# Kernel tuning notes

Hardware: AMD Instinct MI355X
Metric: run time of the kernel (lower is better)

Reference implementation:

```python
import jax, jax.numpy as jnp
import numpy as np

E = 1024
H = 16
D = E // H  # head_dim = 64
B, L, S = 2, 2048, 2048


def setup_inputs() -> dict:
    key = jax.random.key(0)
    ks = jax.random.split(key, 10)
    scale = 1.0 / np.sqrt(E)
    return {
        "x": jax.random.normal(ks[0], (B, L, E), jnp.float32),
        "context": jax.random.normal(ks[1], (B, S, E), jnp.float32),
        "Wq": jax.random.normal(ks[2], (E, E), jnp.float32) * scale,
        "bq": jnp.zeros((E,), jnp.float32),
        "Wk": jax.random.normal(ks[3], (E, E), jnp.float32) * scale,
        "bk": jnp.zeros((E,), jnp.float32),
        "Wv": jax.random.normal(ks[4], (E, E), jnp.float32) * scale,
        "bv": jnp.zeros((E,), jnp.float32),
        "Wp": jax.random.normal(ks[5], (E, E), jnp.float32) * scale,
        "bp": jnp.zeros((E,), jnp.float32),
    }


def reference(x, context, Wq, bq, Wk, bk, Wv, bv, Wp, bp):
    b, l, _ = x.shape
    s = context.shape[1]
    # linear projections then split heads: [B, H, L/S, D]
    q = (x @ Wq + bq).reshape(b, l, H, D).transpose(0, 2, 1, 3)
    k = (context @ Wk + bk).reshape(b, s, H, D).transpose(0, 2, 1, 3)
    v = (context @ Wv + bv).reshape(b, s, H, D).transpose(0, 2, 1, 3)
    # scores [B, H, L, S]
    attn = jnp.einsum("bhld,bhsd->bhls", q, k) / jnp.sqrt(jnp.float32(D))
    attn = jax.nn.softmax(attn, axis=-1)
    # dropout is identity in eval mode
    out = jnp.einsum("bhls,bhsd->bhld", attn, v)
    out = out.transpose(0, 2, 1, 3).reshape(b, l, E)
    return out @ Wp + bp
```

## Files before the change

### kernel.cpp

```cpp
#include <hip/hip_runtime.h>
#include <math.h>

#define B_ 2
#define L_ 2048
#define S_ 2048
#define E_ 1024
#define H_ 16
#define D_ 64
#define SC_ 0.180336880111120f

typedef unsigned short u16;
typedef unsigned int u32;
typedef __attribute__((ext_vector_type(8))) short short8;
typedef __attribute__((ext_vector_type(4))) float floatx4;

__device__ __forceinline__ u16 f2bf(float f) {
    union { float f; unsigned u; } a; a.f = f;
    unsigned r = a.u + 0x7FFFu + ((a.u >> 16) & 1u);
    return (u16)(r >> 16);
}

__device__ __forceinline__ u32 cvt_pk_bf16(float lo, float hi) {
    u32 d;
    asm("v_cvt_pk_bf16_f32 %0, %1, %2" : "=v"(d) : "v"(lo), "v"(hi));
    return d;
}

__device__ __forceinline__ void glds16(const u16* g, u16* l) {
    __builtin_amdgcn_global_load_lds(
        (const __attribute__((address_space(1))) void*)g,
        (__attribute__((address_space(3))) void*)l, 16, 0, 0);
}

__global__ void cast_bf16_kernel(const float* __restrict__ x, const float* __restrict__ ctx,
                                 u16* __restrict__ Xb, u16* __restrict__ Cb) {
    const float* src = blockIdx.y ? ctx : x;
    u16* dst = blockIdx.y ? Cb : Xb;
    int i = blockIdx.x * 256 + threadIdx.x;
    float4 u0 = ((const float4*)src)[2 * i];
    float4 u1 = ((const float4*)src)[2 * i + 1];
    uint4 o;
    o.x = f2bf(u0.x) | ((unsigned)f2bf(u0.y) << 16);
    o.y = f2bf(u0.z) | ((unsigned)f2bf(u0.w) << 16);
    o.z = f2bf(u1.x) | ((unsigned)f2bf(u1.y) << 16);
    o.w = f2bf(u1.z) | ((unsigned)f2bf(u1.w) << 16);
    ((uint4*)dst)[i] = o;
}

__global__ void transpose_cast_kernel(const float* __restrict__ Wq, const float* __restrict__ Wk,
                                      const float* __restrict__ Wv, const float* __restrict__ Wp,
                                      u16* __restrict__ WqT, u16* __restrict__ WkT,
                                      u16* __restrict__ WvT, u16* __restrict__ WpT) {
    const int z = blockIdx.z;
    const float* W = z == 0 ? Wq : (z == 1 ? Wk : (z == 2 ? Wv : Wp));
    u16* Wt = z == 0 ? WqT : (z == 1 ? WkT : (z == 2 ? WvT : WpT));
    __shared__ float tile[32][33];
    const int bx = blockIdx.x * 32, by = blockIdx.y * 32;
    const int tx = threadIdx.x, ty = threadIdx.y;
#pragma unroll
    for (int j = 0; j < 4; ++j)
        tile[ty + j * 8][tx] = W[(size_t)(by + ty + j * 8) * E_ + bx + tx];
    __syncthreads();
#pragma unroll
    for (int j = 0; j < 4; ++j)
        Wt[(size_t)(bx + ty + j * 8) * E_ + by + tx] = f2bf(tile[tx][ty + j * 8]);
}

__global__ __launch_bounds__(256, 3) void qkv_gemm_kernel(
    const u16* __restrict__ Xb, const u16* __restrict__ Cb,
    const u16* __restrict__ WqT, const u16* __restrict__ WkT, const u16* __restrict__ WvT,
    const float* __restrict__ bq, const float* __restrict__ bk, const float* __restrict__ bv,
    u16* __restrict__ Qb, u16* __restrict__ Kb, u16* __restrict__ Vtb) {
    __shared__ __align__(16) u16 As[128 * 64];
    __shared__ __align__(16) u16 Bs[128 * 64];

    const int z = blockIdx.z;
    const u16* A  = z == 0 ? Xb : Cb;
    const u16* Bt = z == 0 ? WqT : (z == 1 ? WkT : WvT);
    const float* bias = z == 0 ? bq : (z == 1 ? bk : bv);
    const float scale = z == 0 ? SC_ : 1.0f;

    const int tid = threadIdx.x;
    const int lane = tid & 63;
    const int wv = tid >> 6;
    const int wm = wv >> 1, wn = wv & 1;
    const int qd = lane >> 4, lr = lane & 15;
    const int m0 = blockIdx.y * 128, n0 = blockIdx.x * 128;
    const int lrow = lane >> 3;
    const int gu = (lane & 7) ^ lrow;

    floatx4 acc[4][4];
#pragma unroll
    for (int i = 0; i < 4; ++i)
#pragma unroll
        for (int j = 0; j < 4; ++j) {
            floatx4 zz = {0.f, 0.f, 0.f, 0.f};
            acc[i][j] = zz;
        }

#pragma unroll
    for (int j = 0; j < 4; ++j) {
        int c = wv * 4 + j;
        glds16(A  + (size_t)(m0 + c * 8 + lrow) * E_ + gu * 8, &As[c * 512]);
        glds16(Bt + (size_t)(n0 + c * 8 + lrow) * E_ + gu * 8, &Bs[c * 512]);
    }
    __syncthreads();

    for (int t = 0; t < 16; ++t) {
        short8 af[4][2], bf[4][2];
#pragma unroll
        for (int mi = 0; mi < 4; ++mi)
#pragma unroll
            for (int kk = 0; kk < 2; ++kk) {
                int row = wm * 64 + mi * 16 + lr;
                int u = (kk * 4 + qd) ^ (lr & 7);
                af[mi][kk] = *(const short8*)(&As[row * 64 + u * 8]);
            }
#pragma unroll
        for (int ni = 0; ni < 4; ++ni)
#pragma unroll
            for (int kk = 0; kk < 2; ++kk) {
                int row = wn * 64 + ni * 16 + lr;
                int u = (kk * 4 + qd) ^ (lr & 7);
                bf[ni][kk] = *(const short8*)(&Bs[row * 64 + u * 8]);
            }
#pragma unroll
        for (int kk = 0; kk < 2; ++kk)
#pragma unroll
            for (int mi = 0; mi < 4; ++mi)
#pragma unroll
                for (int ni = 0; ni < 4; ++ni)
                    acc[mi][ni] = __builtin_amdgcn_mfma_f32_16x16x32_bf16(
                        af[mi][kk], bf[ni][kk], acc[mi][ni], 0, 0, 0);
        __syncthreads();
        if (t + 1 < 16) {
            int kb = (t + 1) * 64;
#pragma unroll
            for (int j = 0; j < 4; ++j) {
                int c = wv * 4 + j;
                glds16(A  + (size_t)(m0 + c * 8 + lrow) * E_ + kb + gu * 8, &As[c * 512]);
                glds16(Bt + (size_t)(n0 + c * 8 + lrow) * E_ + kb + gu * 8, &Bs[c * 512]);
            }
        }
        __syncthreads();
    }

    u16* Cq = z == 0 ? Qb : Kb;
#pragma unroll
    for (int mi = 0; mi < 4; ++mi) {
#pragma unroll
        for (int ni = 0; ni < 4; ++ni) {
            int col = n0 + wn * 64 + ni * 16 + lr;
            float bv_ = bias[col];
            if (z == 2) {
                int row0 = m0 + wm * 64 + mi * 16 + qd * 4;
                int bidx = row0 >> 11;
                int sloc = row0 & (S_ - 1);
                u16 h0 = f2bf(acc[mi][ni][0] + bv_);
                u16 h1 = f2bf(acc[mi][ni][1] + bv_);
                u16 h2 = f2bf(acc[mi][ni][2] + bv_);
                u16 h3 = f2bf(acc[mi][ni][3] + bv_);
                uint2 pk;
                pk.x = h0 | ((unsigned)h1 << 16);
                pk.y = h2 | ((unsigned)h3 << 16);
                *(uint2*)&Vtb[((size_t)(bidx * E_ + col)) * S_ + sloc] = pk;
            } else {
#pragma unroll
                for (int r = 0; r < 4; ++r) {
                    int row = m0 + wm * 64 + mi * 16 + qd * 4 + r;
                    Cq[(size_t)row * E_ + col] = f2bf((acc[mi][ni][r] + bv_) * scale);
                }
            }
        }
    }
}

#define PSTR 68

__global__ __launch_bounds__(256, 4) void flash_attn_kernel(
    const u16* __restrict__ Q, const u16* __restrict__ Kg,
    const u16* __restrict__ Vtg, u16* __restrict__ Opart, float* __restrict__ lpart) {
    __shared__ __align__(16) u16 Ps[128 * PSTR];
    __shared__ __align__(16) u16 Ks[64 * 64];
    __shared__ __align__(16) u16 Vs[64 * 64];

    const int tid = threadIdx.x;
    const int lane = tid & 63;
    const int wv = tid >> 6;
    const int qd = lane >> 4, lr = lane & 15;
    const int b = blockIdx.y >> 4, h = blockIdx.y & 15;
    const int q0 = blockIdx.x * 128;
    const int z = blockIdx.z;
    const int sbeg = z * (S_ / 2);

    u16* Op = Opart + (size_t)z * (B_ * L_ * E_);
    float* lp = lpart + (size_t)z * (B_ * H_ * L_);

    const u16* Qbase = Q + (size_t)(b * L_ + q0) * E_ + h * D_;
    const u16* Kbase = Kg + (size_t)(b * S_) * E_ + h * D_;
    const u16* Vbase = Vtg + (size_t)(b * E_ + h * D_) * S_;

    const int srow = tid >> 3;
    const int scol = (tid & 7) * 8;
    const int lrow = lane >> 3;
    const int gu = (lane & 7) ^ lrow;

#pragma unroll
    for (int j = 0; j < 2; ++j) {
        int c = wv * 2 + j;
        glds16(Kbase + (size_t)(sbeg + c * 8 + lrow) * E_ + gu * 8, &Ks[c * 512]);
        glds16(Vbase + (size_t)(c * 8 + lrow) * S_ + sbeg + gu * 8, &Vs[c * 512]);
    }

#pragma unroll
    for (int c = 0; c < 4; ++c) {
        int row = srow + c * 32;
        *(uint4*)(&Ps[row * PSTR + scol]) = *(const uint4*)(Qbase + (size_t)row * E_ + scol);
    }
    __syncthreads();

    short8 qf[2][2];
#pragma unroll
    for (int mi = 0; mi < 2; ++mi)
#pragma unroll
        for (int kk = 0; kk < 2; ++kk)
            qf[mi][kk] = *(const short8*)(&Ps[(wv * 32 + mi * 16 + lr) * PSTR + kk * 32 + qd * 8]);

    floatx4 o_acc[2][4];
    float l_acc[2][4];
#pragma unroll
    for (int mi = 0; mi < 2; ++mi)
#pragma unroll
        for (int nt = 0; nt < 4; ++nt) {
            floatx4 z4 = {0.f, 0.f, 0.f, 0.f};
            o_acc[mi][nt] = z4;
        }
#pragma unroll
    for (int mi = 0; mi < 2; ++mi)
#pragma unroll
        for (int r = 0; r < 4; ++r) l_acc[mi][r] = 0.f;

    const int NIT = (S_ / 2) / 64;

    for (int it = 0; it < NIT; ++it) {
        floatx4 s_[2][4];
#pragma unroll
        for (int nt = 0; nt < 4; ++nt) {
            int krow = nt * 16 + lr;
            short8 kb0 = *(const short8*)(&Ks[krow * 64 + ((qd) ^ (lr & 7)) * 8]);
            short8 kb1 = *(const short8*)(&Ks[krow * 64 + ((4 + qd) ^ (lr & 7)) * 8]);
#pragma unroll
            for (int mi = 0; mi < 2; ++mi) {
                floatx4 zz = {0.f, 0.f, 0.f, 0.f};
                zz = __builtin_amdgcn_mfma_f32_16x16x32_bf16(qf[mi][0], kb0, zz, 0, 0, 0);
                zz = __builtin_amdgcn_mfma_f32_16x16x32_bf16(qf[mi][1], kb1, zz, 0, 0, 0);
                s_[mi][nt] = zz;
            }
        }

#pragma unroll
        for (int mi = 0; mi < 2; ++mi)
#pragma unroll
            for (int nt = 0; nt < 4; ++nt)
#pragma unroll
                for (int r = 0; r < 4; ++r) {
                    float p = __builtin_amdgcn_exp2f(s_[mi][nt][r]);
                    l_acc[mi][r] += p;
                    Ps[(wv * 32 + mi * 16 + qd * 4 + r) * PSTR + nt * 16 + lr] = f2bf(p);
                }
        asm volatile("s_waitcnt lgkmcnt(0)" ::: "memory");

        short8 pf[2][2];
#pragma unroll
        for (int mi = 0; mi < 2; ++mi)
#pragma unroll
            for (int kk = 0; kk < 2; ++kk)
                pf[mi][kk] = *(const short8*)(&Ps[(wv * 32 + mi * 16 + lr) * PSTR + kk * 32 + qd * 8]);
#pragma unroll
        for (int nt = 0; nt < 4; ++nt) {
            int vrow = nt * 16 + lr;
            short8 vb0 = *(const short8*)(&Vs[vrow * 64 + ((qd) ^ (lr & 7)) * 8]);
            short8 vb1 = *(const short8*)(&Vs[vrow * 64 + ((4 + qd) ^ (lr & 7)) * 8]);
#pragma unroll
            for (int mi = 0; mi < 2; ++mi) {
                o_acc[mi][nt] = __builtin_amdgcn_mfma_f32_16x16x32_bf16(pf[mi][0], vb0, o_acc[mi][nt], 0, 0, 0);
                o_acc[mi][nt] = __builtin_amdgcn_mfma_f32_16x16x32_bf16(pf[mi][1], vb1, o_acc[mi][nt], 0, 0, 0);
            }
        }

        __syncthreads();
        if (it + 1 < NIT) {
            int s1 = sbeg + (it + 1) * 64;
#pragma unroll
            for (int j = 0; j < 2; ++j) {
                int c = wv * 2 + j;
                glds16(Kbase + (size_t)(s1 + c * 8 + lrow) * E_ + gu * 8, &Ks[c * 512]);
                glds16(Vbase + (size_t)(c * 8 + lrow) * S_ + s1 + gu * 8, &Vs[c * 512]);
            }
            __syncthreads();
        }
    }

    float linv[2][4];
#pragma unroll
    for (int mi = 0; mi < 2; ++mi)
#pragma unroll
        for (int r = 0; r < 4; ++r) {
            float l = l_acc[mi][r];
#pragma unroll
            for (int st = 1; st < 16; st <<= 1) l += __shfl_xor(l, st);
            if (lr == 0)
                lp[(size_t)(b * H_ + h) * L_ + q0 + wv * 32 + mi * 16 + qd * 4 + r] = l;
            linv[mi][r] = 1.0f / l;
        }

#pragma unroll
    for (int mi = 0; mi < 2; ++mi)
#pragma unroll
        for (int nt = 0; nt < 4; ++nt)
#pragma unroll
            for (int r = 0; r < 4; ++r) {
                int row = q0 + wv * 32 + mi * 16 + qd * 4 + r;
                int col = h * D_ + nt * 16 + lr;
                Op[(size_t)(b * L_ + row) * E_ + col] = f2bf(o_acc[mi][nt][r] * linv[mi][r]);
            }
}

__global__ __launch_bounds__(256, 2) void out_gemm_kernel(
    const u16* __restrict__ O1, const u16* __restrict__ O2,
    const float* __restrict__ l1, const float* __restrict__ l2,
    const u16* __restrict__ WpT, const float* __restrict__ bp,
    float* __restrict__ out) {
    __shared__ __align__(16) u16 As[128 * 64];
    __shared__ __align__(16) u16 Bs[128 * 64];

    const int tid = threadIdx.x;
    const int lane = tid & 63;
    const int wv = tid >> 6;
    const int wm = wv >> 1, wn = wv & 1;
    const int qd = lane >> 4, lr = lane & 15;
    const int m0 = blockIdx.y * 128, n0 = blockIdx.x * 128;
    const int lrow = lane >> 3;
    const int gu = (lane & 7) ^ lrow;

    floatx4 acc[4][4];
#pragma unroll
    for (int i = 0; i < 4; ++i)
#pragma unroll
        for (int j = 0; j < 4; ++j) {
            floatx4 zz = {0.f, 0.f, 0.f, 0.f};
            acc[i][j] = zz;
        }

#define STAGE_A(tt)                                                                   \
    {                                                                                 \
        int col = (tt)*64 + gu * 8;                                                   \
        _Pragma("unroll") for (int j = 0; j < 4; ++j) {                               \
            int c = wv * 4 + j;                                                       \
            int row = m0 + c * 8 + lrow;                                              \
            uint4 a1 = *(const uint4*)(O1 + (size_t)row * E_ + col);                  \
            uint4 a2 = *(const uint4*)(O2 + (size_t)row * E_ + col);                  \
            int li = (row >> 11) * (H_ * L_) + (tt)*L_ + (row & (L_ - 1));            \
            float la = l1[li], lb = l2[li];                                           \
            float s = 1.0f / (la + lb);                                               \
            float w1 = la * s, w2 = lb * s;                                           \
            const u32* pa = (const u32*)&a1;                                          \
            const u32* pb = (const u32*)&a2;                                          \
            uint4 o;                                                                  \
            u32* po = (u32*)&o;                                                       \
            _Pragma("unroll") for (int d = 0; d < 4; ++d) {                           \
                union { u32 u; float f; } x0, x1, y0, y1;                             \
                x0.u = pa[d] << 16; x1.u = pa[d] & 0xFFFF0000u;                       \
                y0.u = pb[d] << 16; y1.u = pb[d] & 0xFFFF0000u;                       \
                po[d] = cvt_pk_bf16(x0.f * w1 + y0.f * w2, x1.f * w1 + y1.f * w2);    \
            }                                                                         \
            *(uint4*)(&As[c * 512 + lane * 8]) = o;                                   \
        }                                                                             \
    }

#pragma unroll
    for (int j = 0; j < 4; ++j) {
        int c = wv * 4 + j;
        glds16(WpT + (size_t)(n0 + c * 8 + lrow) * E_ + gu * 8, &Bs[c * 512]);
    }
    STAGE_A(0)
    __syncthreads();

    for (int t = 0; t < 16; ++t) {
        short8 af[4][2], bf[4][2];
#pragma unroll
        for (int mi = 0; mi < 4; ++mi)
#pragma unroll
            for (int kk = 0; kk < 2; ++kk) {
                int row = wm * 64 + mi * 16 + lr;
                int u = (kk * 4 + qd) ^ (lr & 7);
                af[mi][kk] = *(const short8*)(&As[row * 64 + u * 8]);
            }
#pragma unroll
        for (int ni = 0; ni < 4; ++ni)
#pragma unroll
            for (int kk = 0; kk < 2; ++kk) {
                int row = wn * 64 + ni * 16 + lr;
                int u = (kk * 4 + qd) ^ (lr & 7);
                bf[ni][kk] = *(const short8*)(&Bs[row * 64 + u * 8]);
            }
#pragma unroll
        for (int kk = 0; kk < 2; ++kk)
#pragma unroll
            for (int mi = 0; mi < 4; ++mi)
#pragma unroll
                for (int ni = 0; ni < 4; ++ni)
                    acc[mi][ni] = __builtin_amdgcn_mfma_f32_16x16x32_bf16(
                        af[mi][kk], bf[ni][kk], acc[mi][ni], 0, 0, 0);
        __syncthreads();
        if (t + 1 < 16) {
            int kb = (t + 1) * 64;
#pragma unroll
            for (int j = 0; j < 4; ++j) {
                int c = wv * 4 + j;
                glds16(WpT + (size_t)(n0 + c * 8 + lrow) * E_ + kb + gu * 8, &Bs[c * 512]);
            }
            STAGE_A(t + 1)
        }
        __syncthreads();
    }

#pragma unroll
    for (int mi = 0; mi < 4; ++mi)
#pragma unroll
        for (int ni = 0; ni < 4; ++ni) {
            int col = n0 + wn * 64 + ni * 16 + lr;
            float bv_ = bp[col];
#pragma unroll
            for (int r = 0; r < 4; ++r) {
                int row = m0 + wm * 64 + mi * 16 + qd * 4 + r;
                out[(size_t)row * E_ + col] = acc[mi][ni][r] + bv_;
            }
        }
}

extern "C" void kernel_launch(void* const* d_in, const int* in_sizes, int n_in,
                              void* d_out, int out_size, void* d_ws, size_t ws_size,
                              hipStream_t stream) {
    const float* x   = (const float*)d_in[0];
    const float* ctx = (const float*)d_in[1];
    const float* Wq  = (const float*)d_in[2];
    const float* bq  = (const float*)d_in[3];
    const float* Wk  = (const float*)d_in[4];
    const float* bk  = (const float*)d_in[5];
    const float* Wv  = (const float*)d_in[6];
    const float* bv  = (const float*)d_in[7];
    const float* Wp  = (const float*)d_in[8];
    const float* bp  = (const float*)d_in[9];
    float* out = (float*)d_out;

    u16* WqT = (u16*)d_ws;
    u16* WkT = WqT + 1048576;
    u16* WvT = WkT + 1048576;
    u16* WpT = WvT + 1048576;
    u16* Qb  = WpT + 1048576;
    u16* Kb  = Qb + 4194304;
    u16* Vtb = Kb + 4194304;
    u16* Xb  = Vtb + 4194304;
    u16* Cb  = Xb + 4194304;
    u16* Opart = Xb;
    float* lpart = (float*)(Cb + 4194304);
    (void)ws_size; (void)in_sizes; (void)n_in; (void)out_size;

    cast_bf16_kernel<<<dim3(2048, 2), 256, 0, stream>>>(x, ctx, Xb, Cb);
    transpose_cast_kernel<<<dim3(32, 32, 4), dim3(32, 8), 0, stream>>>(
        Wq, Wk, Wv, Wp, WqT, WkT, WvT, WpT);

    qkv_gemm_kernel<<<dim3(8, 32, 3), 256, 0, stream>>>(
        Xb, Cb, WqT, WkT, WvT, bq, bk, bv, Qb, Kb, Vtb);

    flash_attn_kernel<<<dim3(L_ / 128, B_ * H_, 2), 256, 0, stream>>>(
        Qb, Kb, Vtb, Opart, lpart);

    out_gemm_kernel<<<dim3(8, 32), 256, 0, stream>>>(
        Opart, Opart + 4194304, lpart, lpart + B_ * H_ * L_, WpT, bp, out);
}
```

Measured before the change: 242.4 us.

## Double-buffer LDS tiles in all GEMM and attention kernels, fuse input cast into QKV

Drops the separate fp32-to-bf16 cast kernel for x and context. The QKV GEMM now reads fp32 activations directly into registers and converts them into a double-buffered LDS tile. The QKV GEMM, flash attention and output GEMM all move to two LDS buffers, so the next tile's loads are issued before the current tile's MFMAs, and each iteration needs one barrier instead of two. This trades larger LDS and register footprint (occupancy hints lowered from 3→2 and 4→3) for overlap of memory with compute and one fewer kernel launch and round trip through global memory.

```diff
diff --git a/kernel.cpp b/kernel.cpp
--- a/kernel.cpp
+++ b/kernel.cpp
@@ -30,21 +30,6 @@
     __builtin_amdgcn_global_load_lds(
         (const __attribute__((address_space(1))) void*)g,
         (__attribute__((address_space(3))) void*)l, 16, 0, 0);
-}
-
-__global__ void cast_bf16_kernel(const float* __restrict__ x, const float* __restrict__ ctx,
-                                 u16* __restrict__ Xb, u16* __restrict__ Cb) {
-    const float* src = blockIdx.y ? ctx : x;
-    u16* dst = blockIdx.y ? Cb : Xb;
-    int i = blockIdx.x * 256 + threadIdx.x;
-    float4 u0 = ((const float4*)src)[2 * i];
-    float4 u1 = ((const float4*)src)[2 * i + 1];
-    uint4 o;
-    o.x = f2bf(u0.x) | ((unsigned)f2bf(u0.y) << 16);
-    o.y = f2bf(u0.z) | ((unsigned)f2bf(u0.w) << 16);
-    o.z = f2bf(u1.x) | ((unsigned)f2bf(u1.y) << 16);
-    o.w = f2bf(u1.z) | ((unsigned)f2bf(u1.w) << 16);
-    ((uint4*)dst)[i] = o;
 }
 
 __global__ void transpose_cast_kernel(const float* __restrict__ Wq, const float* __restrict__ Wk,
@@ -66,16 +51,16 @@
         Wt[(size_t)(bx + ty + j * 8) * E_ + by + tx] = f2bf(tile[tx][ty + j * 8]);
 }
 
-__global__ __launch_bounds__(256, 3) void qkv_gemm_kernel(
-    const u16* __restrict__ Xb, const u16* __restrict__ Cb,
+__global__ __launch_bounds__(256, 2) void qkv_gemm_kernel(
+    const float* __restrict__ x, const float* __restrict__ ctx,
     const u16* __restrict__ WqT, const u16* __restrict__ WkT, const u16* __restrict__ WvT,
     const float* __restrict__ bq, const float* __restrict__ bk, const float* __restrict__ bv,
     u16* __restrict__ Qb, u16* __restrict__ Kb, u16* __restrict__ Vtb) {
-    __shared__ __align__(16) u16 As[128 * 64];
-    __shared__ __align__(16) u16 Bs[128 * 64];
+    __shared__ __align__(16) u16 As[2][128 * 64];
+    __shared__ __align__(16) u16 Bs[2][128 * 64];
 
     const int z = blockIdx.z;
-    const u16* A  = z == 0 ? Xb : Cb;
+    const float* A  = z == 0 ? x : ctx;
     const u16* Bt = z == 0 ? WqT : (z == 1 ? WkT : WvT);
     const float* bias = z == 0 ? bq : (z == 1 ? bk : bv);
     const float scale = z == 0 ? SC_ : 1.0f;
@@ -88,6 +73,8 @@
     const int m0 = blockIdx.y * 128, n0 = blockIdx.x * 128;
     const int lrow = lane >> 3;
     const int gu = (lane & 7) ^ lrow;
+    const int arow = tid >> 3;
+    const int au = tid & 7;
 
     floatx4 acc[4][4];
 #pragma unroll
@@ -98,15 +85,51 @@
             acc[i][j] = zz;
         }
 
-#pragma unroll
-    for (int j = 0; j < 4; ++j) {
-        int c = wv * 4 + j;
-        glds16(A  + (size_t)(m0 + c * 8 + lrow) * E_ + gu * 8, &As[c * 512]);
-        glds16(Bt + (size_t)(n0 + c * 8 + lrow) * E_ + gu * 8, &Bs[c * 512]);
-    }
+    float4 av[4][2];
+
+#define LOAD_A(kb)                                                                 \
+    {                                                                              \
+        _Pragma("unroll") for (int c2 = 0; c2 < 4; ++c2) {                         \
+            const float* src = A + (size_t)(m0 + arow + c2 * 32) * E_ + (kb) + au * 8; \
+            av[c2][0] = *(const float4*)src;                                       \
+            av[c2][1] = *(const float4*)(src + 4);                                 \
+        }                                                                          \
+    }
+
+#define WRITE_A(buf)                                                               \
+    {                                                                              \
+        _Pragma("unroll") for (int c2 = 0; c2 < 4; ++c2) {                         \
+            int row = arow + c2 * 32;                                              \
+            uint4 o;                                                               \
+            o.x = cvt_pk_bf16(av[c2][0].x, av[c2][0].y);                           \
+            o.y = cvt_pk_bf16(av[c2][0].z, av[c2][0].w);                           \
+            o.z = cvt_pk_bf16(av[c2][1].x, av[c2][1].y);                           \
+            o.w = cvt_pk_bf16(av[c2][1].z, av[c2][1].w);                           \
+            *(uint4*)(&As[buf][row * 64 + (au ^ (row & 7)) * 8]) = o;              \
+        }                                                                          \
+    }
+
+#define STAGE_B(buf, kb)                                                           \
+    {                                                                              \
+        _Pragma("unroll") for (int j = 0; j < 4; ++j) {                            \
+            int c = wv * 4 + j;                                                    \
+            glds16(Bt + (size_t)(n0 + c * 8 + lrow) * E_ + (kb) + gu * 8,          \
+                   &Bs[buf][c * 512]);                                             \
+        }                                                                          \
+    }
+
+    LOAD_A(0)
+    STAGE_B(0, 0)
+    WRITE_A(0)
     __syncthreads();
 
     for (int t = 0; t < 16; ++t) {
+        const int cur = t & 1;
+        if (t + 1 < 16) {
+            STAGE_B(cur ^ 1, (t + 1) * 64)
+            LOAD_A((t + 1) * 64)
+        }
+
         short8 af[4][2], bf[4][2];
 #pragma unroll
         for (int mi = 0; mi < 4; ++mi)
@@ -114,7 +137,7 @@
             for (int kk = 0; kk < 2; ++kk) {
                 int row = wm * 64 + mi * 16 + lr;
                 int u = (kk * 4 + qd) ^ (lr & 7);
-                af[mi][kk] = *(const short8*)(&As[row * 64 + u * 8]);
+                af[mi][kk] = *(const short8*)(&As[cur][row * 64 + u * 8]);
             }
 #pragma unroll
         for (int ni = 0; ni < 4; ++ni)
@@ -122,7 +145,7 @@
             for (int kk = 0; kk < 2; ++kk) {
                 int row = wn * 64 + ni * 16 + lr;
                 int u = (kk * 4 + qd) ^ (lr & 7);
-                bf[ni][kk] = *(const short8*)(&Bs[row * 64 + u * 8]);
+                bf[ni][kk] = *(const short8*)(&Bs[cur][row * 64 + u * 8]);
             }
 #pragma unroll
         for (int kk = 0; kk < 2; ++kk)
@@ -132,16 +155,8 @@
                 for (int ni = 0; ni < 4; ++ni)
                     acc[mi][ni] = __builtin_amdgcn_mfma_f32_16x16x32_bf16(
                         af[mi][kk], bf[ni][kk], acc[mi][ni], 0, 0, 0);
-        __syncthreads();
-        if (t + 1 < 16) {
-            int kb = (t + 1) * 64;
-#pragma unroll
-            for (int j = 0; j < 4; ++j) {
-                int c = wv * 4 + j;
-                glds16(A  + (size_t)(m0 + c * 8 + lrow) * E_ + kb + gu * 8, &As[c * 512]);
-                glds16(Bt + (size_t)(n0 + c * 8 + lrow) * E_ + kb + gu * 8, &Bs[c * 512]);
-            }
-        }
+
+        if (t + 1 < 16) WRITE_A(cur ^ 1)
         __syncthreads();
     }
 
@@ -173,16 +188,19 @@
             }
         }
     }
+#undef LOAD_A
+#undef WRITE_A
+#undef STAGE_B
 }
 
 #define PSTR 68
 
-__global__ __launch_bounds__(256, 4) void flash_attn_kernel(
+__global__ __launch_bounds__(256, 3) void flash_attn_kernel(
     const u16* __restrict__ Q, const u16* __restrict__ Kg,
     const u16* __restrict__ Vtg, u16* __restrict__ Opart, float* __restrict__ lpart) {
     __shared__ __align__(16) u16 Ps[128 * PSTR];
-    __shared__ __align__(16) u16 Ks[64 * 64];
-    __shared__ __align__(16) u16 Vs[64 * 64];
+    __shared__ __align__(16) u16 Ks[2][64 * 64];
+    __shared__ __align__(16) u16 Vs[2][64 * 64];
 
     const int tid = threadIdx.x;
     const int lane = tid & 63;
@@ -208,8 +226,8 @@
 #pragma unroll
     for (int j = 0; j < 2; ++j) {
         int c = wv * 2 + j;
-        glds16(Kbase + (size_t)(sbeg + c * 8 + lrow) * E_ + gu * 8, &Ks[c * 512]);
-        glds16(Vbase + (size_t)(c * 8 + lrow) * S_ + sbeg + gu * 8, &Vs[c * 512]);
+        glds16(Kbase + (size_t)(sbeg + c * 8 + lrow) * E_ + gu * 8, &Ks[0][c * 512]);
+        glds16(Vbase + (size_t)(c * 8 + lrow) * S_ + sbeg + gu * 8, &Vs[0][c * 512]);
     }
 
 #pragma unroll
@@ -243,12 +261,23 @@
     const int NIT = (S_ / 2) / 64;
 
     for (int it = 0; it < NIT; ++it) {
+        const int cur = it & 1;
+        if (it + 1 < NIT) {
+            int s1 = sbeg + (it + 1) * 64;
+#pragma unroll
+            for (int j = 0; j < 2; ++j) {
+                int c = wv * 2 + j;
+                glds16(Kbase + (size_t)(s1 + c * 8 + lrow) * E_ + gu * 8, &Ks[cur ^ 1][c * 512]);
+                glds16(Vbase + (size_t)(c * 8 + lrow) * S_ + s1 + gu * 8, &Vs[cur ^ 1][c * 512]);
+            }
+        }
+
         floatx4 s_[2][4];
 #pragma unroll
         for (int nt = 0; nt < 4; ++nt) {
             int krow = nt * 16 + lr;
-            short8 kb0 = *(const short8*)(&Ks[krow * 64 + ((qd) ^ (lr & 7)) * 8]);
-            short8 kb1 = *(const short8*)(&Ks[krow * 64 + ((4 + qd) ^ (lr & 7)) * 8]);
+            short8 kb0 = *(const short8*)(&Ks[cur][krow * 64 + ((qd) ^ (lr & 7)) * 8]);
+            short8 kb1 = *(const short8*)(&Ks[cur][krow * 64 + ((4 + qd) ^ (lr & 7)) * 8]);
 #pragma unroll
             for (int mi = 0; mi < 2; ++mi) {
                 floatx4 zz = {0.f, 0.f, 0.f, 0.f};
@@ -279,8 +308,8 @@
 #pragma unroll
         for (int nt = 0; nt < 4; ++nt) {
             int vrow = nt * 16 + lr;
-            short8 vb0 = *(const short8*)(&Vs[vrow * 64 + ((qd) ^ (lr & 7)) * 8]);
-            short8 vb1 = *(const short8*)(&Vs[vrow * 64 + ((4 + qd) ^ (lr & 7)) * 8]);
+            short8 vb0 = *(const short8*)(&Vs[cur][vrow * 64 + ((qd) ^ (lr & 7)) * 8]);
+            short8 vb1 = *(const short8*)(&Vs[cur][vrow * 64 + ((4 + qd) ^ (lr & 7)) * 8]);
 #pragma unroll
             for (int mi = 0; mi < 2; ++mi) {
                 o_acc[mi][nt] = __builtin_amdgcn_mfma_f32_16x16x32_bf16(pf[mi][0], vb0, o_acc[mi][nt], 0, 0, 0);
@@ -289,16 +318,6 @@
         }
 
         __syncthreads();
-        if (it + 1 < NIT) {
-            int s1 = sbeg + (it + 1) * 64;
-#pragma unroll
-            for (int j = 0; j < 2; ++j) {
-                int c = wv * 2 + j;
-                glds16(Kbase + (size_t)(s1 + c * 8 + lrow) * E_ + gu * 8, &Ks[c * 512]);
-                glds16(Vbase + (size_t)(c * 8 + lrow) * S_ + s1 + gu * 8, &Vs[c * 512]);
-            }
-            __syncthreads();
-        }
     }
 
     float linv[2][4];
@@ -331,8 +350,8 @@
     const float* __restrict__ l1, const float* __restrict__ l2,
     const u16* __restrict__ WpT, const float* __restrict__ bp,
     float* __restrict__ out) {
-    __shared__ __align__(16) u16 As[128 * 64];
-    __shared__ __align__(16) u16 Bs[128 * 64];
+    __shared__ __align__(16) u16 As[2][128 * 64];
+    __shared__ __align__(16) u16 Bs[2][128 * 64];
 
     const int tid = threadIdx.x;
     const int lane = tid & 63;
@@ -352,41 +371,64 @@
             acc[i][j] = zz;
         }
 
-#define STAGE_A(tt)                                                                   \
-    {                                                                                 \
-        int col = (tt)*64 + gu * 8;                                                   \
-        _Pragma("unroll") for (int j = 0; j < 4; ++j) {                               \
-            int c = wv * 4 + j;                                                       \
-            int row = m0 + c * 8 + lrow;                                              \
-            uint4 a1 = *(const uint4*)(O1 + (size_t)row * E_ + col);                  \
-            uint4 a2 = *(const uint4*)(O2 + (size_t)row * E_ + col);                  \
-            int li = (row >> 11) * (H_ * L_) + (tt)*L_ + (row & (L_ - 1));            \
-            float la = l1[li], lb = l2[li];                                           \
-            float s = 1.0f / (la + lb);                                               \
-            float w1 = la * s, w2 = lb * s;                                           \
-            const u32* pa = (const u32*)&a1;                                          \
-            const u32* pb = (const u32*)&a2;                                          \
-            uint4 o;                                                                  \
-            u32* po = (u32*)&o;                                                       \
-            _Pragma("unroll") for (int d = 0; d < 4; ++d) {                           \
-                union { u32 u; float f; } x0, x1, y0, y1;                             \
-                x0.u = pa[d] << 16; x1.u = pa[d] & 0xFFFF0000u;                       \
-                y0.u = pb[d] << 16; y1.u = pb[d] & 0xFFFF0000u;                       \
-                po[d] = cvt_pk_bf16(x0.f * w1 + y0.f * w2, x1.f * w1 + y1.f * w2);    \
-            }                                                                         \
-            *(uint4*)(&As[c * 512 + lane * 8]) = o;                                   \
-        }                                                                             \
-    }
-
-#pragma unroll
-    for (int j = 0; j < 4; ++j) {
-        int c = wv * 4 + j;
-        glds16(WpT + (size_t)(n0 + c * 8 + lrow) * E_ + gu * 8, &Bs[c * 512]);
-    }
-    STAGE_A(0)
+    uint4 p1[4], p2[4];
+    float la_[4], lb_[4];
+
+#define LOAD_AO(tt)                                                                \
+    {                                                                              \
+        _Pragma("unroll") for (int j = 0; j < 4; ++j) {                            \
+            int c = wv * 4 + j;                                                    \
+            int row = m0 + c * 8 + lrow;                                           \
+            int col = (tt)*64 + gu * 8;                                            \
+            p1[j] = *(const uint4*)(O1 + (size_t)row * E_ + col);                  \
+            p2[j] = *(const uint4*)(O2 + (size_t)row * E_ + col);                  \
+            int li = (row >> 11) * (H_ * L_) + (tt)*L_ + (row & (L_ - 1));         \
+            la_[j] = l1[li];                                                       \
+            lb_[j] = l2[li];                                                       \
+        }                                                                          \
+    }
+
+#define WRITE_AO(buf)                                                              \
+    {                                                                              \
+        _Pragma("unroll") for (int j = 0; j < 4; ++j) {                            \
+            int c = wv * 4 + j;                                                    \
+            float s = 1.0f / (la_[j] + lb_[j]);                                    \
+            float w1 = la_[j] * s, w2 = lb_[j] * s;                                \
+            const u32* pa = (const u32*)&p1[j];                                    \
+            const u32* pb = (const u32*)&p2[j];                                    \
+            uint4 o;                                                               \
+            u32* po = (u32*)&o;                                                    \
+            _Pragma("unroll") for (int d = 0; d < 4; ++d) {                        \
+                union { u32 u; float f; } x0, x1, y0, y1;                          \
+                x0.u = pa[d] << 16; x1.u = pa[d] & 0xFFFF0000u;                    \
+                y0.u = pb[d] << 16; y1.u = pb[d] & 0xFFFF0000u;                    \
+                po[d] = cvt_pk_bf16(x0.f * w1 + y0.f * w2, x1.f * w1 + y1.f * w2); \
+            }                                                                      \
+            *(uint4*)(&As[buf][c * 512 + lane * 8]) = o;                           \
+        }                                                                          \
+    }
+
+#define STAGE_BO(buf, kb)                                                          \
+    {                                                                              \
+        _Pragma("unroll") for (int j = 0; j < 4; ++j) {                            \
+            int c = wv * 4 + j;                                                    \
+            glds16(WpT + (size_t)(n0 + c * 8 + lrow) * E_ + (kb) + gu * 8,         \
+                   &Bs[buf][c * 512]);                                             \
+        }                                                                          \
+    }
+
+    LOAD_AO(0)
+    STAGE_BO(0, 0)
+    WRITE_AO(0)
     __syncthreads();
 
     for (int t = 0; t < 16; ++t) {
+        const int cur = t & 1;
+        if (t + 1 < 16) {
+            STAGE_BO(cur ^ 1, (t + 1) * 64)
+            LOAD_AO(t + 1)
+        }
+
         short8 af[4][2], bf[4][2];
 #pragma unroll
         for (int mi = 0; mi < 4; ++mi)
@@ -394,7 +436,7 @@
             for (int kk = 0; kk < 2; ++kk) {
                 int row = wm * 64 + mi * 16 + lr;
                 int u = (kk * 4 + qd) ^ (lr & 7);
-                af[mi][kk] = *(const short8*)(&As[row * 64 + u * 8]);
+                af[mi][kk] = *(const short8*)(&As[cur][row * 64 + u * 8]);
             }
 #pragma unroll
         for (int ni = 0; ni < 4; ++ni)
@@ -402,7 +444,7 @@
             for (int kk = 0; kk < 2; ++kk) {
                 int row = wn * 64 + ni * 16 + lr;
                 int u = (kk * 4 + qd) ^ (lr & 7);
-                bf[ni][kk] = *(const short8*)(&Bs[row * 64 + u * 8]);
+                bf[ni][kk] = *(const short8*)(&Bs[cur][row * 64 + u * 8]);
             }
 #pragma unroll
         for (int kk = 0; kk < 2; ++kk)
@@ -412,16 +454,8 @@
                 for (int ni = 0; ni < 4; ++ni)
                     acc[mi][ni] = __builtin_amdgcn_mfma_f32_16x16x32_bf16(
                         af[mi][kk], bf[ni][kk], acc[mi][ni], 0, 0, 0);
-        __syncthreads();
-        if (t + 1 < 16) {
-            int kb = (t + 1) * 64;
-#pragma unroll
-            for (int j = 0; j < 4; ++j) {
-                int c = wv * 4 + j;
-                glds16(WpT + (size_t)(n0 + c * 8 + lrow) * E_ + kb + gu * 8, &Bs[c * 512]);
-            }
-            STAGE_A(t + 1)
-        }
+
+        if (t + 1 < 16) WRITE_AO(cur ^ 1)
         __syncthreads();
     }
 
@@ -437,6 +471,9 @@
                 out[(size_t)row * E_ + col] = acc[mi][ni][r] + bv_;
             }
         }
+#undef LOAD_AO
+#undef WRITE_AO
+#undef STAGE_BO
 }
 
 extern "C" void kernel_launch(void* const* d_in, const int* in_sizes, int n_in,
@@ -461,18 +498,15 @@
     u16* Qb  = WpT + 1048576;
     u16* Kb  = Qb + 4194304;
     u16* Vtb = Kb + 4194304;
-    u16* Xb  = Vtb + 4194304;
-    u16* Cb  = Xb + 4194304;
-    u16* Opart = Xb;
-    float* lpart = (float*)(Cb + 4194304);
+    u16* Opart = Vtb + 4194304;
+    float* lpart = (float*)(Opart + 2 * 4194304);
     (void)ws_size; (void)in_sizes; (void)n_in; (void)out_size;
 
-    cast_bf16_kernel<<<dim3(2048, 2), 256, 0, stream>>>(x, ctx, Xb, Cb);
     transpose_cast_kernel<<<dim3(32, 32, 4), dim3(32, 8), 0, stream>>>(
         Wq, Wk, Wv, Wp, WqT, WkT, WvT, WpT);
 
     qkv_gemm_kernel<<<dim3(8, 32, 3), 256, 0, stream>>>(
-        Xb, Cb, WqT, WkT, WvT, bq, bk, bv, Qb, Kb, Vtb);
+        x, ctx, WqT, WkT, WvT, bq, bk, bv, Qb, Kb, Vtb);
 
     flash_attn_kernel<<<dim3(L_ / 128, B_ * H_, 2), 256, 0, stream>>>(
         Qb, Kb, Vtb, Opart, lpart);
```

Result: slower. 280.3 us (+15.6%).
